# Kernel optimization log

Hardware: AMD Instinct MI355X
Metric: run time of the kernel (lower is better)

The kernel has to match this reference:

```python
import jax, jax.numpy as jnp
import numpy as np

B, S, D = 2, 2048, 2048
H, Dh = 16, 128  # qkv_features = H*Dh = 2048
NEG = -1e10


def setup_inputs() -> dict:
    key = jax.random.key(0)
    k1, k2, k3 = jax.random.split(key, 3)
    x = jax.random.normal(k1, (B, S, D), dtype=jnp.float32)
    # variance_scaling(1.0, 'fan_in', 'normal') ~ std = 1/sqrt(fan_in)
    Wqkv = jax.random.normal(k2, (D, 3 * H * Dh), dtype=jnp.float32) / np.sqrt(D)
    bqkv = jnp.zeros((3 * H * Dh,), dtype=jnp.float32)
    Wout = jax.random.normal(k3, (H * Dh, D), dtype=jnp.float32) / np.sqrt(H * Dh)
    bout = jnp.zeros((D,), dtype=jnp.float32)
    return {"x": x, "Wqkv": Wqkv, "bqkv": bqkv, "Wout": Wout, "bout": bout}


def reference(x, Wqkv, bqkv, Wout, bout):
    b, s, _ = x.shape
    # fused QKV projection
    qkv = x @ Wqkv + bqkv                                   # [B, S, 3*H*Dh]
    qkv = qkv.reshape(b, s, 3, H, Dh).transpose(2, 0, 3, 1, 4)  # [3, B, H, S, Dh]
    q, k, v = qkv[0], qkv[1], qkv[2]
    scale = 1.0 / jnp.sqrt(jnp.asarray(Dh, dtype=x.dtype))
    # Each query chunk attends to the full key sequence with a causal mask,
    # which is mathematically full causal attention.
    scores = jnp.einsum('bhqd,bhkd->bhqk', q, k) * scale    # [B, H, S, S]
    causal = jnp.arange(s)[None, :] <= jnp.arange(s)[:, None]  # k <= q
    scores = jnp.where(causal[None, None, :, :], scores, NEG)
    weights = jax.nn.softmax(scores, axis=-1)
    out = jnp.einsum('bhqk,bhkd->bhqd', weights, v)         # [B, H, S, Dh]
    out = out.transpose(0, 2, 1, 3).reshape(b, s, H * Dh)
    return out @ Wout + bout
```

## Files before the change

### kernel.cpp

```cpp
#include <hip/hip_runtime.h>


typedef unsigned short u16;
typedef __attribute__((ext_vector_type(8))) short bf16x8;
typedef __attribute__((ext_vector_type(4))) float f32x4;

#define MFMA(a, b, c) __builtin_amdgcn_mfma_f32_16x16x32_bf16((a), (b), (c), 0, 0, 0)

__device__ __forceinline__ u16 f2bf(float f) {
    unsigned u = __builtin_bit_cast(unsigned, f);
    u += 0x7fffu + ((u >> 16) & 1u);
    return (u16)(u >> 16);
}

__device__ __forceinline__ void gload16(const void* g, void* l) {
    __builtin_amdgcn_global_load_lds(
        (const __attribute__((address_space(1))) void*)g,
        (__attribute__((address_space(3))) void*)l, 16, 0, 0);
}


__global__ __launch_bounds__(256) void k_cast(const float* __restrict__ src,
                                              u16* __restrict__ dst, int n4) {
    int i = blockIdx.x * 256 + threadIdx.x;
    if (i >= n4) return;
    float4 a = ((const float4*)src)[i];
    ushort4 r;
    r.x = f2bf(a.x); r.y = f2bf(a.y); r.z = f2bf(a.z); r.w = f2bf(a.w);
    ((ushort4*)dst)[i] = r;
}

__global__ __launch_bounds__(256) void k_castT(const float* __restrict__ src,
                                               u16* __restrict__ dst, int rows, int cols) {
    __shared__ float t[32][33];
    int c0 = blockIdx.x * 32, r0 = blockIdx.y * 32;
    int tx = threadIdx.x, ty = threadIdx.y;
#pragma unroll
    for (int i = 0; i < 4; ++i)
        t[ty + 8 * i][tx] = src[(size_t)(r0 + ty + 8 * i) * cols + (c0 + tx)];
    __syncthreads();
#pragma unroll
    for (int i = 0; i < 4; ++i)
        dst[(size_t)(c0 + ty + 8 * i) * rows + (r0 + tx)] = f2bf(t[tx][ty + 8 * i]);
}

__global__ __launch_bounds__(256) void k_transv(const u16* __restrict__ v,
                                                u16* __restrict__ vT) {
    __shared__ u16 t[32][33];
    int head = blockIdx.z;
    int s0 = blockIdx.x * 32, d0 = blockIdx.y * 32;
    const u16* vp = v + (size_t)head * 2048 * 128;
    u16* op = vT + (size_t)head * 128 * 2048;
    int tx = threadIdx.x, ty = threadIdx.y;
#pragma unroll
    for (int i = 0; i < 4; ++i)
        t[ty + 8 * i][tx] = vp[(size_t)(s0 + ty + 8 * i) * 128 + d0 + tx];
    __syncthreads();
#pragma unroll
    for (int i = 0; i < 4; ++i)
        op[(size_t)(d0 + ty + 8 * i) * 2048 + (s0 + tx)] = t[tx][ty + 8 * i];
}


template <int K>
__device__ __forceinline__ void gemm_core(const u16* __restrict__ A,
                                          const u16* __restrict__ BT,
                                          int m0, int n0,
                                          f32x4 (&acc)[4][4],
                                          u16* As, u16* Bs) {
    const int tid = threadIdx.x, wave = tid >> 6, lane = tid & 63;
    const int wr = (wave >> 1) * 64, wc = (wave & 1) * 64;
    for (int k0 = 0; k0 < K; k0 += 32) {
        __syncthreads();
#pragma unroll
        for (int i = 0; i < 2; ++i) {
            int cb = (i * 4 + wave) * 64;
            int c = cb + lane;
            int row = c >> 2, kk = (c & 3) * 8;
            gload16(A + (size_t)(m0 + row) * K + k0 + kk, As + cb * 8);
            gload16(BT + (size_t)(n0 + row) * K + k0 + kk, Bs + cb * 8);
        }
        __syncthreads();
        bf16x8 a[4], b[4];
#pragma unroll
        for (int m = 0; m < 4; ++m)
            a[m] = *(const bf16x8*)(As + (wr + m * 16 + (lane & 15)) * 32 + (lane >> 4) * 8);
#pragma unroll
        for (int n = 0; n < 4; ++n)
            b[n] = *(const bf16x8*)(Bs + (wc + n * 16 + (lane & 15)) * 32 + (lane >> 4) * 8);
        __builtin_amdgcn_s_setprio(1);
#pragma unroll
        for (int m = 0; m < 4; ++m)
#pragma unroll
            for (int n = 0; n < 4; ++n)
                acc[m][n] = MFMA(a[m], b[n], acc[m][n]);
        __builtin_amdgcn_s_setprio(0);
    }
}

__global__ __launch_bounds__(256) void k_gemm_qkv(const u16* __restrict__ A,
                                                  const u16* __restrict__ BT,
                                                  const float* __restrict__ bias,
                                                  u16* __restrict__ q,
                                                  u16* __restrict__ kbuf,
                                                  u16* __restrict__ v) {
    __shared__ __align__(16) u16 As[128 * 32];
    __shared__ __align__(16) u16 Bs[128 * 32];
    f32x4 acc[4][4] = {};
    const int orig = blockIdx.y * 48 + blockIdx.x;
    const int nb = (orig & 7) * 192 + (orig >> 3);
    const int m0 = (nb / 48) * 128, n0 = (nb % 48) * 128;
    gemm_core<2048>(A, BT, m0, n0, acc, As, Bs);

    const int tid = threadIdx.x, wave = tid >> 6, lane = tid & 63;
    const int wr = (wave >> 1) * 64, wc = (wave & 1) * 64;
    const int t = n0 >> 11;
    u16* dst = (t == 0) ? q : (t == 1) ? kbuf : v;
#pragma unroll
    for (int m = 0; m < 4; ++m)
#pragma unroll
        for (int n = 0; n < 4; ++n)
#pragma unroll
            for (int j = 0; j < 4; ++j) {
                int gr = m0 + wr + m * 16 + (lane >> 4) * 4 + j;
                int gc = n0 + wc + n * 16 + (lane & 15);
                float val = acc[m][n][j] + bias[gc];
                int bb = gr >> 11, s = gr & 2047;
                int rem = gc & 2047, h = rem >> 7, d = rem & 127;
                dst[((size_t)(bb * 16 + h) * 2048 + s) * 128 + d] = f2bf(val);
            }
}

__global__ __launch_bounds__(256) void k_gemm_out(const u16* __restrict__ A,
                                                  const u16* __restrict__ BT,
                                                  const float* __restrict__ bias,
                                                  float* __restrict__ out) {
    __shared__ __align__(16) u16 As[128 * 32];
    __shared__ __align__(16) u16 Bs[128 * 32];
    f32x4 acc[4][4] = {};
    const int orig = blockIdx.y * 16 + blockIdx.x;
    const int nb = (orig & 7) * 64 + (orig >> 3);
    const int m0 = (nb / 16) * 128, n0 = (nb % 16) * 128;
    gemm_core<2048>(A, BT, m0, n0, acc, As, Bs);

    const int tid = threadIdx.x, wave = tid >> 6, lane = tid & 63;
    const int wr = (wave >> 1) * 64, wc = (wave & 1) * 64;
#pragma unroll
    for (int m = 0; m < 4; ++m)
#pragma unroll
        for (int n = 0; n < 4; ++n)
#pragma unroll
            for (int j = 0; j < 4; ++j) {
                int gr = m0 + wr + m * 16 + (lane >> 4) * 4 + j;
                int gc = n0 + wc + n * 16 + (lane & 15);
                out[(size_t)gr * 2048 + gc] = acc[m][n][j] + bias[gc];
            }
}

__global__ __launch_bounds__(256) void k_attn(const u16* __restrict__ q,
                                              const u16* __restrict__ k,
                                              const u16* __restrict__ vT,
                                              u16* __restrict__ o) {
    __shared__ __align__(16) u16 KsA[2 * 64 * 128];
    __shared__ __align__(16) u16 VsA[2 * 128 * 64];
    __shared__ __align__(16) u16 PsA[4 * 16 * 64];
    char* ksB = (char*)KsA;
    char* vsB = (char*)VsA;

    const int tid = threadIdx.x, wave = tid >> 6, lane = tid & 63;
    char* psB = (char*)PsA + wave * 2048;

    const int lin = blockIdx.x;
    const int dd = (lin & 7) * 64 + (lin >> 3);
    const int head = dd >> 4, pair = dd & 15;

    const u16* qh = q + (size_t)head * 2048 * 128;
    const u16* kh = k + (size_t)head * 2048 * 128;
    const u16* vh = vT + (size_t)head * 128 * 2048;
    const int bb = head >> 4, hh = head & 15;
    const float qscale = 0.1275293562566334f;

    bf16x8 ones;
#pragma unroll
    for (int e = 0; e < 8; ++e) ones[e] = (short)0x3F80;

    auto stage = [&](int kv0, int bufsel) {
        char* kd = ksB + bufsel * 16384;
        char* vd = vsB + bufsel * 16384;
#pragma unroll
        for (int i = 0; i < 4; ++i) {
            int cb = (i * 4 + wave) * 64;
            int d = (cb + lane) * 16;
            int r = d >> 8;
            int co = (d & 255) ^ ((r & 7) << 4);
            gload16(kh + (size_t)(kv0 + r) * 128 + (co >> 1), kd + cb * 16);
        }
#pragma unroll
        for (int i = 0; i < 4; ++i) {
            int cb = (i * 4 + wave) * 64;
            int d = (cb + lane) * 16;
            int vr = d >> 7;
            int co = (d & 127) ^ ((vr & 7) << 4);
            gload16(vh + (size_t)vr * 2048 + kv0 + (co >> 1), vd + cb * 16);
        }
    };

#pragma unroll 1
    for (int qsel = 0; qsel < 2; ++qsel) {
        const int qi = qsel ? (31 - pair) : pair;
        const int q0 = qi * 64;
        const int ntile = qi + 1;

        bf16x8 qf[4];
        const int qr = q0 + wave * 16 + (lane & 15);
#pragma unroll
        for (int kt = 0; kt < 4; ++kt)
            qf[kt] = *(const bf16x8*)(qh + (size_t)qr * 128 + kt * 32 + (lane >> 4) * 8);

        f32x4 o_acc[8] = {};
        float m_r[4], l_r[4];
#pragma unroll
        for (int j = 0; j < 4; ++j) { m_r[j] = -1e30f; l_r[j] = 0.f; }

        stage(0, 0);
        int buf = 0;

#pragma unroll 1
        for (int t = 0; t < ntile; ++t) {
            const int kv0 = t * 64;
            if (t + 1 < ntile) {
                stage(kv0 + 64, buf ^ 1);
                asm volatile("s_waitcnt vmcnt(8)" ::: "memory");
            } else {
                asm volatile("s_waitcnt vmcnt(0)" ::: "memory");
            }
            __builtin_amdgcn_s_barrier();
            char* kb_ = ksB + buf * 16384;
            char* vb_ = vsB + buf * 16384;

            f32x4 s_acc[4] = {};
            __builtin_amdgcn_s_setprio(1);
#pragma unroll
            for (int c = 0; c < 4; ++c) {
                int row = c * 16 + (lane & 15);
#pragma unroll
                for (int kt = 0; kt < 4; ++kt) {
                    bf16x8 kbf = *(const bf16x8*)(kb_ +
                        ((row * 256 + kt * 64 + (lane >> 4) * 16) ^ ((row & 7) << 4)));
                    s_acc[c] = MFMA(qf[kt], kbf, s_acc[c]);
                }
            }
            __builtin_amdgcn_s_setprio(0);

            const bool maskblk = (kv0 + 64 > q0);
            float bm[4];
#pragma unroll
            for (int j = 0; j < 4; ++j) {
                int qg = q0 + wave * 16 + (lane >> 4) * 4 + j;
                float mx = -1e30f;
#pragma unroll
                for (int c = 0; c < 4; ++c) {
                    float sv = s_acc[c][j] * qscale;
                    if (maskblk && (kv0 + c * 16 + (lane & 15)) > qg) sv = -1e30f;
                    s_acc[c][j] = sv;
                    mx = fmaxf(mx, sv);
                }
#pragma unroll
                for (int t2 = 1; t2 < 16; t2 <<= 1) mx = fmaxf(mx, __shfl_xor(mx, t2));
                bm[j] = mx;
            }
            bool grow = (bm[0] > m_r[0] + 8.f) | (bm[1] > m_r[1] + 8.f) |
                        (bm[2] > m_r[2] + 8.f) | (bm[3] > m_r[3] + 8.f);
            if (__any(grow)) {
#pragma unroll
                for (int j = 0; j < 4; ++j) {
                    float mnew = fmaxf(m_r[j], bm[j]);
                    float al = exp2f(m_r[j] - mnew);
                    m_r[j] = mnew;
                    l_r[j] *= al;
#pragma unroll
                    for (int c2 = 0; c2 < 8; ++c2) o_acc[c2][j] *= al;
                }
            }
#pragma unroll
            for (int j = 0; j < 4; ++j)
#pragma unroll
                for (int c = 0; c < 4; ++c)
                    s_acc[c][j] = exp2f(s_acc[c][j] - m_r[j]);

#pragma unroll
            for (int c = 0; c < 4; ++c)
#pragma unroll
                for (int j = 0; j < 4; ++j) {
                    int row = (lane >> 4) * 4 + j;
                    *(u16*)(psB + ((row * 128 + (c * 16 + (lane & 15)) * 2) ^ ((row & 7) << 4)))
                        = f2bf(s_acc[c][j]);
                }
            bf16x8 pf[2];
#pragma unroll
            for (int kt = 0; kt < 2; ++kt) {
                int row2 = lane & 15;
                pf[kt] = *(const bf16x8*)(psB +
                    ((row2 * 128 + kt * 64 + (lane >> 4) * 16) ^ ((row2 & 7) << 4)));
            }

            __builtin_amdgcn_s_setprio(1);
            f32x4 rs_acc = {};
            rs_acc = MFMA(pf[0], ones, rs_acc);
            rs_acc = MFMA(pf[1], ones, rs_acc);
#pragma unroll
            for (int c2 = 0; c2 < 8; ++c2) {
#pragma unroll
                for (int kt = 0; kt < 2; ++kt) {
                    int row = c2 * 16 + (lane & 15);
                    bf16x8 vf = *(const bf16x8*)(vb_ +
                        ((row * 128 + kt * 64 + (lane >> 4) * 16) ^ ((row & 7) << 4)));
                    o_acc[c2] = MFMA(pf[kt], vf, o_acc[c2]);
                }
            }
            __builtin_amdgcn_s_setprio(0);
#pragma unroll
            for (int j = 0; j < 4; ++j) l_r[j] += rs_acc[j];

            __builtin_amdgcn_s_barrier();
            buf ^= 1;
        }

        float linv[4];
#pragma unroll
        for (int j = 0; j < 4; ++j) linv[j] = 1.0f / l_r[j];
#pragma unroll
        for (int c2 = 0; c2 < 8; ++c2)
#pragma unroll
            for (int j = 0; j < 4; ++j) {
                int qg = q0 + wave * 16 + (lane >> 4) * 4 + j;
                int d2 = c2 * 16 + (lane & 15);
                o[((size_t)(bb * 2048 + qg)) * 2048 + hh * 128 + d2]
                    = f2bf(o_acc[c2][j] * linv[j]);
            }
    }
}


extern "C" void kernel_launch(void* const* d_in, const int* in_sizes, int n_in,
                              void* d_out, int out_size, void* d_ws, size_t ws_size,
                              hipStream_t stream) {
    const float* x    = (const float*)d_in[0];
    const float* Wqkv = (const float*)d_in[1];
    const float* bqkv = (const float*)d_in[2];
    const float* Wout = (const float*)d_in[3];
    const float* bout = (const float*)d_in[4];
    float* out = (float*)d_out;

    char* ws = (char*)d_ws;
    const size_t SZ = 16777216;
    u16* q   = (u16*)(ws);
    u16* kb  = (u16*)(ws + SZ);
    u16* v   = (u16*)(ws + 2 * SZ);
    u16* vT  = (u16*)(ws + 3 * SZ);
    u16* ao  = v;
    u16* xb  = (u16*)(ws + 4 * SZ);
    u16* WqT = (u16*)(ws + 5 * SZ);
    u16* WoT = (u16*)(ws + 5 * SZ + 25165824);

    k_cast<<<dim3(8192), dim3(256), 0, stream>>>(x, xb, 2097152);
    k_castT<<<dim3(192, 64), dim3(32, 8), 0, stream>>>(Wqkv, WqT, 2048, 6144);
    k_castT<<<dim3(64, 64), dim3(32, 8), 0, stream>>>(Wout, WoT, 2048, 2048);
    k_gemm_qkv<<<dim3(48, 32), dim3(256), 0, stream>>>(xb, WqT, bqkv, q, kb, v);
    k_transv<<<dim3(64, 4, 32), dim3(32, 8), 0, stream>>>(v, vT);
    k_attn<<<dim3(512), dim3(256), 0, stream>>>(q, kb, vT, ao);
    k_gemm_out<<<dim3(16, 32), dim3(256), 0, stream>>>(ao, WoT, bout, out);
}
```

Measured before the change: 296.7 us.

## Rewrite projection GEMMs as 8-wave 128x256 tiles with double-buffered swizzled LDS

Both projection GEMMs now use 512-thread blocks computing 128x256 tiles with a K-step of 64. The A and B tiles are double-buffered in XOR-swizzled LDS, and the next tile's global-to-LDS loads are interleaved with four MFMA phases using explicit waitcnt and barriers. This aims to hide global-load latency, cut LDS bank conflicts and raise data reuse per block. In exchange it uses 96KB of LDS per block, which limits occupancy, and it relies on fragile hand-written waitcnt and barrier ordering.

```diff
diff --git a/kernel.cpp b/kernel.cpp
--- a/kernel.cpp
+++ b/kernel.cpp
@@ -63,57 +63,148 @@
 
 
 template <int K>
-__device__ __forceinline__ void gemm_core(const u16* __restrict__ A,
-                                          const u16* __restrict__ BT,
-                                          int m0, int n0,
-                                          f32x4 (&acc)[4][4],
-                                          u16* As, u16* Bs) {
+__device__ __forceinline__ void gemm8_core(const u16* __restrict__ A,
+                                           const u16* __restrict__ BT,
+                                           int m0, int n0,
+                                           f32x4 (&acc)[4][4],
+                                           char* AsB, char* BsB) {
     const int tid = threadIdx.x, wave = tid >> 6, lane = tid & 63;
-    const int wr = (wave >> 1) * 64, wc = (wave & 1) * 64;
-    for (int k0 = 0; k0 < K; k0 += 32) {
-        __syncthreads();
+    const int wr = (wave >> 2) * 64, wc = (wave & 3) * 64;
+
+    auto stageA = [&](int kt, int buf) {
+        char* dst = AsB + buf * 16384;
+        const u16* src = A + (size_t)m0 * K + kt * 64;
 #pragma unroll
         for (int i = 0; i < 2; ++i) {
-            int cb = (i * 4 + wave) * 64;
-            int c = cb + lane;
-            int row = c >> 2, kk = (c & 3) * 8;
-            gload16(A + (size_t)(m0 + row) * K + k0 + kk, As + cb * 8);
-            gload16(BT + (size_t)(n0 + row) * K + k0 + kk, Bs + cb * 8);
+            int cb = wave * 128 + i * 64;
+            int d = (cb + lane) * 16;
+            int r = d >> 7, col = (d & 127) ^ ((r & 7) << 4);
+            gload16(src + (size_t)r * K + (col >> 1), dst + cb * 16);
         }
-        __syncthreads();
-        bf16x8 a[4], b[4];
-#pragma unroll
-        for (int m = 0; m < 4; ++m)
-            a[m] = *(const bf16x8*)(As + (wr + m * 16 + (lane & 15)) * 32 + (lane >> 4) * 8);
-#pragma unroll
-        for (int n = 0; n < 4; ++n)
-            b[n] = *(const bf16x8*)(Bs + (wc + n * 16 + (lane & 15)) * 32 + (lane >> 4) * 8);
+    };
+    auto stageB = [&](int kt, int buf, int ih) {
+        char* dst = BsB + buf * 32768;
+        const u16* src = BT + (size_t)n0 * K + kt * 64;
+#pragma unroll
+        for (int i = 0; i < 2; ++i) {
+            int cb = wave * 256 + (ih * 2 + i) * 64;
+            int d = (cb + lane) * 16;
+            int r = d >> 7, col = (d & 127) ^ ((r & 7) << 4);
+            gload16(src + (size_t)r * K + (col >> 1), dst + cb * 16);
+        }
+    };
+    auto ldA = [&](int m, int kk, int buf) -> bf16x8 {
+        int row = wr + m * 16 + (lane & 15);
+        int byte = (row * 128 + kk * 64 + (lane >> 4) * 16) ^ ((row & 7) << 4);
+        return *(const bf16x8*)(AsB + buf * 16384 + byte);
+    };
+    auto ldB = [&](int n, int kk, int buf) -> bf16x8 {
+        int row = wc + n * 16 + (lane & 15);
+        int byte = (row * 128 + kk * 64 + (lane >> 4) * 16) ^ ((row & 7) << 4);
+        return *(const bf16x8*)(BsB + buf * 32768 + byte);
+    };
+
+    stageA(0, 0); stageB(0, 0, 0); stageB(0, 0, 1);
+
+    bf16x8 afr[2][2];
+    bf16x8 bfr[4][2];
+    const int NT = K / 64;
+#pragma unroll 1
+    for (int t = 0; t < NT; ++t) {
+        const int buf = t & 1;
+        const bool pre = (t + 1 < NT);
+
+        if (pre) stageA(t + 1, buf ^ 1);
+        if (pre) asm volatile("s_waitcnt vmcnt(2)" ::: "memory");
+        else     asm volatile("s_waitcnt vmcnt(0)" ::: "memory");
+        __builtin_amdgcn_s_barrier();
+#pragma unroll
+        for (int m = 0; m < 2; ++m)
+#pragma unroll
+            for (int kk = 0; kk < 2; ++kk) afr[m][kk] = ldA(m, kk, buf);
+#pragma unroll
+        for (int n = 0; n < 2; ++n)
+#pragma unroll
+            for (int kk = 0; kk < 2; ++kk) bfr[n][kk] = ldB(n, kk, buf);
+        asm volatile("s_waitcnt lgkmcnt(0)" ::: "memory");
+        __builtin_amdgcn_sched_barrier(0);
         __builtin_amdgcn_s_setprio(1);
 #pragma unroll
-        for (int m = 0; m < 4; ++m)
-#pragma unroll
-            for (int n = 0; n < 4; ++n)
-                acc[m][n] = MFMA(a[m], b[n], acc[m][n]);
+        for (int m = 0; m < 2; ++m)
+#pragma unroll
+            for (int n = 0; n < 2; ++n)
+#pragma unroll
+                for (int kk = 0; kk < 2; ++kk)
+                    acc[m][n] = MFMA(afr[m][kk], bfr[n][kk], acc[m][n]);
+        __builtin_amdgcn_s_setprio(0);
+        __builtin_amdgcn_s_barrier();
+
+#pragma unroll
+        for (int n = 0; n < 2; ++n)
+#pragma unroll
+            for (int kk = 0; kk < 2; ++kk) bfr[2 + n][kk] = ldB(2 + n, kk, buf);
+        if (pre) stageB(t + 1, buf ^ 1, 0);
+        __builtin_amdgcn_s_barrier();
+        asm volatile("s_waitcnt lgkmcnt(0)" ::: "memory");
+        __builtin_amdgcn_sched_barrier(0);
+        __builtin_amdgcn_s_setprio(1);
+#pragma unroll
+        for (int m = 0; m < 2; ++m)
+#pragma unroll
+            for (int n = 0; n < 2; ++n)
+#pragma unroll
+                for (int kk = 0; kk < 2; ++kk)
+                    acc[m][2 + n] = MFMA(afr[m][kk], bfr[2 + n][kk], acc[m][2 + n]);
+        __builtin_amdgcn_s_setprio(0);
+        __builtin_amdgcn_s_barrier();
+
+#pragma unroll
+        for (int m = 0; m < 2; ++m)
+#pragma unroll
+            for (int kk = 0; kk < 2; ++kk) afr[m][kk] = ldA(2 + m, kk, buf);
+        if (pre) stageB(t + 1, buf ^ 1, 1);
+        __builtin_amdgcn_s_barrier();
+        asm volatile("s_waitcnt lgkmcnt(0)" ::: "memory");
+        __builtin_amdgcn_sched_barrier(0);
+        __builtin_amdgcn_s_setprio(1);
+#pragma unroll
+        for (int m = 0; m < 2; ++m)
+#pragma unroll
+            for (int n = 0; n < 2; ++n)
+#pragma unroll
+                for (int kk = 0; kk < 2; ++kk)
+                    acc[2 + m][n] = MFMA(afr[m][kk], bfr[n][kk], acc[2 + m][n]);
+        __builtin_amdgcn_s_setprio(0);
+        __builtin_amdgcn_s_barrier();
+
+        __builtin_amdgcn_s_setprio(1);
+#pragma unroll
+        for (int m = 0; m < 2; ++m)
+#pragma unroll
+            for (int n = 0; n < 2; ++n)
+#pragma unroll
+                for (int kk = 0; kk < 2; ++kk)
+                    acc[2 + m][2 + n] = MFMA(afr[m][kk], bfr[2 + n][kk], acc[2 + m][2 + n]);
         __builtin_amdgcn_s_setprio(0);
     }
 }
 
-__global__ __launch_bounds__(256) void k_gemm_qkv(const u16* __restrict__ A,
+__global__ __launch_bounds__(512) void k_gemm_qkv(const u16* __restrict__ A,
                                                   const u16* __restrict__ BT,
                                                   const float* __restrict__ bias,
                                                   u16* __restrict__ q,
                                                   u16* __restrict__ kbuf,
                                                   u16* __restrict__ v) {
-    __shared__ __align__(16) u16 As[128 * 32];
-    __shared__ __align__(16) u16 Bs[128 * 32];
+    __shared__ __align__(16) char AsB[2 * 16384];
+    __shared__ __align__(16) char BsB[2 * 32768];
     f32x4 acc[4][4] = {};
-    const int orig = blockIdx.y * 48 + blockIdx.x;
-    const int nb = (orig & 7) * 192 + (orig >> 3);
-    const int m0 = (nb / 48) * 128, n0 = (nb % 48) * 128;
-    gemm_core<2048>(A, BT, m0, n0, acc, As, Bs);
+    const int orig = blockIdx.x;
+    const int dd = (orig & 7) * 96 + (orig >> 3);
+    const int m0 = (dd / 24) * 128, n0 = (dd % 24) * 256;
+    gemm8_core<2048>(A, BT, m0, n0, acc, AsB, BsB);
 
     const int tid = threadIdx.x, wave = tid >> 6, lane = tid & 63;
-    const int wr = (wave >> 1) * 64, wc = (wave & 1) * 64;
+    const int wr = (wave >> 2) * 64, wc = (wave & 3) * 64;
     const int t = n0 >> 11;
     u16* dst = (t == 0) ? q : (t == 1) ? kbuf : v;
 #pragma unroll
@@ -131,20 +222,20 @@
             }
 }
 
-__global__ __launch_bounds__(256) void k_gemm_out(const u16* __restrict__ A,
+__global__ __launch_bounds__(512) void k_gemm_out(const u16* __restrict__ A,
                                                   const u16* __restrict__ BT,
                                                   const float* __restrict__ bias,
                                                   float* __restrict__ out) {
-    __shared__ __align__(16) u16 As[128 * 32];
-    __shared__ __align__(16) u16 Bs[128 * 32];
+    __shared__ __align__(16) char AsB[2 * 16384];
+    __shared__ __align__(16) char BsB[2 * 32768];
     f32x4 acc[4][4] = {};
-    const int orig = blockIdx.y * 16 + blockIdx.x;
-    const int nb = (orig & 7) * 64 + (orig >> 3);
-    const int m0 = (nb / 16) * 128, n0 = (nb % 16) * 128;
-    gemm_core<2048>(A, BT, m0, n0, acc, As, Bs);
+    const int orig = blockIdx.x;
+    const int dd = (orig & 7) * 32 + (orig >> 3);
+    const int m0 = (dd / 8) * 128, n0 = (dd % 8) * 256;
+    gemm8_core<2048>(A, BT, m0, n0, acc, AsB, BsB);
 
     const int tid = threadIdx.x, wave = tid >> 6, lane = tid & 63;
-    const int wr = (wave >> 1) * 64, wc = (wave & 1) * 64;
+    const int wr = (wave >> 2) * 64, wc = (wave & 3) * 64;
 #pragma unroll
     for (int m = 0; m < 4; ++m)
 #pragma unroll
@@ -366,8 +457,8 @@
     k_cast<<<dim3(8192), dim3(256), 0, stream>>>(x, xb, 2097152);
     k_castT<<<dim3(192, 64), dim3(32, 8), 0, stream>>>(Wqkv, WqT, 2048, 6144);
     k_castT<<<dim3(64, 64), dim3(32, 8), 0, stream>>>(Wout, WoT, 2048, 2048);
-    k_gemm_qkv<<<dim3(48, 32), dim3(256), 0, stream>>>(xb, WqT, bqkv, q, kb, v);
+    k_gemm_qkv<<<dim3(768), dim3(512), 0, stream>>>(xb, WqT, bqkv, q, kb, v);
     k_transv<<<dim3(64, 4, 32), dim3(32, 8), 0, stream>>>(v, vT);
     k_attn<<<dim3(512), dim3(256), 0, stream>>>(q, kb, vT, ao);
-    k_gemm_out<<<dim3(16, 32), dim3(256), 0, stream>>>(ao, WoT, bout, out);
-}
+    k_gemm_out<<<dim3(256), dim3(512), 0, stream>>>(ao, WoT, bout, out);
+}
```

After: 319.2 us. +7.6%, slower.
